# Performance work log

Measured on AMD Instinct MI355X. Metric: run time of the kernel, lower is better.

## Reference

```python
import jax, jax.numpy as jnp
import numpy as np

B, S, IN_DIM, OUT_DIM = 4, 2048, 1024, 1024
NEG = -9e15

def _xavier(key, shape, gain=1.414):
    fan_in, fan_out = shape[0], shape[1]
    a = gain * np.sqrt(6.0 / (fan_in + fan_out))
    return jax.random.uniform(key, shape, jnp.float32, -a, a)

def setup_inputs() -> dict:
    key = jax.random.key(0)
    ks = jax.random.split(key, 8)
    x = jax.random.normal(ks[0], (B, S, IN_DIM), jnp.float32)
    W_query = _xavier(ks[1], (IN_DIM, OUT_DIM))
    W_key = _xavier(ks[2], (IN_DIM, OUT_DIM))
    W_value = _xavier(ks[3], (IN_DIM, OUT_DIM))
    # torch Linear default init (kaiming-uniform-ish); values don't matter for correctness baseline
    W1 = _xavier(ks[4], (OUT_DIM + IN_DIM, OUT_DIM), gain=1.0)
    b1 = jnp.zeros((OUT_DIM,), jnp.float32)
    W2 = _xavier(ks[5], (OUT_DIM, OUT_DIM), gain=1.0)
    b2 = jnp.zeros((OUT_DIM,), jnp.float32)
    return {"x": x, "W_query": W_query, "W_key": W_key, "W_value": W_value,
            "W1": W1, "b1": b1, "W2": W2, "b2": b2}

def reference(x, W_query, W_key, W_value, W1, b1, W2, b2):
    # QKV projections: [B,S,in] @ [in,out] -> [B,S,out]
    q = jnp.einsum('bsi,io->bso', x, W_query)
    k = jnp.einsum('bsi,io->bso', x, W_key)
    v = jnp.einsum('bsi,io->bso', x, W_value)
    scale = 1.0 / jnp.sqrt(jnp.float32(OUT_DIM))
    e = jnp.einsum('bqd,bkd->bqk', q, k) * scale  # [B,S,S]
    causal = jnp.tril(jnp.ones((S, S), jnp.float32))  # mask > 0 keeps lower triangle
    attn = jnp.where(causal > 0, e, jnp.float32(NEG))
    attn = jax.nn.softmax(attn, axis=2)
    # dropout: eval mode (train=False) -> identity
    out = jnp.einsum('bqk,bkd->bqd', attn, v)  # [B,S,out]
    h = jnp.concatenate([out, x], axis=-1)  # [B,S,out+in]
    h = jax.nn.relu(jnp.einsum('bsf,fo->bso', h, W1) + b1)
    return jnp.einsum('bsf,fo->bso', h, W2) + b2
```

## Files before the change

kernel.cpp:

```cpp
#include <hip/hip_runtime.h>
#include <stdint.h>

typedef __attribute__((ext_vector_type(8))) short short8;
typedef __attribute__((ext_vector_type(4))) short short4v;
typedef __attribute__((ext_vector_type(4))) float f32x4;

__device__ __forceinline__ unsigned short f32_to_bf16(float f) {
    unsigned int u = __float_as_uint(f);
    u += 0x7FFFu + ((u >> 16) & 1u);
    return (unsigned short)(u >> 16);
}

__device__ __forceinline__ short8 load8_f32_as_bf16(const float* __restrict__ ap) {
    f32x4 f0 = *(const f32x4*)ap;
    f32x4 f1 = *(const f32x4*)(ap + 4);
    union { short8 s; unsigned short u[8]; } cv;
#pragma unroll
    for (int t = 0; t < 4; ++t) {
        cv.u[t]     = f32_to_bf16(f0[t]);
        cv.u[t + 4] = f32_to_bf16(f1[t]);
    }
    return cv.s;
}

__device__ __forceinline__ void gld_lds16(const void* g, void* l) {
    __builtin_amdgcn_global_load_lds(
        (const __attribute__((address_space(1))) unsigned int*)(unsigned long long)(uintptr_t)g,
        (__attribute__((address_space(3))) unsigned int*)(unsigned int)(uintptr_t)l,
        16, 0, 0);
}

template<int EPI, int SWIZ, int MT>
__global__ __launch_bounds__(256, 4)
void gemm128(const unsigned short* __restrict__ A,
             int lda,
             const unsigned short* __restrict__ B, int ldb,
             void* __restrict__ C, int ldc, int K,
             long bStride, long cStride,
             void* __restrict__ C2, int ldc2)
{
    int z = blockIdx.z;
    int mblk, nblk;
    {
        int x = blockIdx.x, yy = blockIdx.y;
        if (z < 2) { mblk = x * 8 + (yy & 7); nblk = yy >> 3; }
        else       { nblk = x * 8 + (yy & 7); mblk = yy >> 3; }
    }
    int m0 = mblk * MT;
    int n0 = nblk * 128;

    const unsigned short* Ab;
    const unsigned short* Bb;
    if (z < 2) { Ab = A; Bb = B + (size_t)z * bStride; }
    else       { Ab = B + (size_t)2 * bStride; Bb = A; }

    __shared__ __align__(16) short As[MT * 64];
    __shared__ __align__(16) short Bs[128 * 64];

    int tid  = threadIdx.x;
    int lane = tid & 63, wid = tid >> 6;
    constexpr int MI = MT / 32;
    int wm = (wid & 1) * (MT / 2), wn = (wid >> 1) * 64;
    int fr = lane & 15, fq = lane >> 4;
    int sw0 = ((fq    ) ^ (fr & 7)) * 16;
    int sw1 = ((fq ^ 4) ^ (fr & 7)) * 16;

    int rS = tid >> 3;
    int cS = ((tid & 7) ^ (rS & 7)) * 8;
    char* AsB = (char*)As; char* BsB = (char*)Bs;

    f32x4 acc[MI][4];
#pragma unroll
    for (int i = 0; i < MI; ++i)
#pragma unroll
    for (int j = 0; j < 4; ++j) acc[i][j] = f32x4{0.f, 0.f, 0.f, 0.f};

    for (int k0 = 0; k0 < K; k0 += 64) {
        const unsigned short* pa = Ab + (size_t)(m0 + rS) * lda + k0 + cS;
        const unsigned short* pb = Bb + (size_t)(n0 + rS) * ldb + k0 + cS;
#pragma unroll
        for (int t = 0; t < MT / 32; ++t)
            gld_lds16(pa + (size_t)(32 * t) * lda, AsB + t * 4096 + tid * 16);
#pragma unroll
        for (int t = 0; t < 4; ++t)
            gld_lds16(pb + (size_t)(32 * t) * ldb,  BsB + t * 4096 + tid * 16);
        __syncthreads();

#pragma unroll
        for (int kh = 0; kh < 2; ++kh) {
            int sw = kh ? sw1 : sw0;
            short8 a[MI], b[4];
#pragma unroll
            for (int i = 0; i < MI; ++i)
                a[i] = *(const short8*)(AsB + (wm + i * 16 + fr) * 128 + sw);
#pragma unroll
            for (int j = 0; j < 4; ++j)
                b[j] = *(const short8*)(BsB + (wn + j * 16 + fr) * 128 + sw);
#pragma unroll
            for (int i = 0; i < MI; ++i)
#pragma unroll
            for (int j = 0; j < 4; ++j)
                acc[i][j] = __builtin_amdgcn_mfma_f32_16x16x32_bf16(a[i], b[j], acc[i][j], 0, 0, 0);
        }
        __syncthreads();
    }

    unsigned short* Cz; int ldcz;
    if (z >= 2) { Cz = (unsigned short*)C2; ldcz = ldc2; }
    else { Cz = (unsigned short*)C + (size_t)z * cStride; ldcz = ldc; }
#pragma unroll
    for (int i = 0; i < MI; ++i)
#pragma unroll
    for (int j = 0; j < 4; ++j)
#pragma unroll
    for (int r = 0; r < 4; ++r) {
        int row = m0 + wm + i * 16 + fq * 4 + r;
        int col = n0 + wn + j * 16 + fr;
        Cz[(size_t)row * ldcz + col] = f32_to_bf16(acc[i][j][r]);
    }
}

template<int AMODE, int EPI, int SWIZ, bool KLIMIT>
__global__ __launch_bounds__(512, 2)
void gemm8p(const unsigned short* __restrict__ A, const unsigned short* __restrict__ A2,
            int lda, int lda2, int ksplit,
            const unsigned short* __restrict__ B, int ldb,
            void* __restrict__ C, int ldc, int K,
            long aStride, long bStride, long cStride,
            const float* __restrict__ bias, long biasStride, float scale)
{
    int z = blockIdx.z;
    int mblk, nblk;
    if (SWIZ == 1) {
        int lin = blockIdx.y * gridDim.x + blockIdx.x;
        int xcd = lin & 7, idx = lin >> 3;
        int mch = (int)gridDim.y >> 3;
        mblk = xcd * mch + idx % mch;
        nblk = idx / mch;
    } else if (SWIZ == 5) {
        int x = blockIdx.x;
        int i = 0;
        while (i < 7 && (i + 1) * (i + 2) <= x) ++i;
        mblk = i;
        nblk = x - i * (i + 1);
    } else if (SWIZ == 8) {
        int p = blockIdx.x;
        int s = (int)blockIdx.z * 8 + (int)blockIdx.y;
        nblk = s >> 2;
        int msel = (s >> 1) & 1, zsel = s & 1;
        z    = 2 * (p & 1) + zsel;
        mblk = msel ? 7 - (p >> 1) : (p >> 1);
    } else {
        mblk = blockIdx.y;
        nblk = blockIdx.x;
    }
    int m0 = mblk * 256, n0 = nblk * 128;

    const unsigned short* Ab = A + (size_t)z * aStride;
    const unsigned short* Bb = B + (size_t)z * bStride;

    constexpr int TILE = 49152;
    __shared__ __align__(16) char lds[3 * TILE];

    int tid  = threadIdx.x;
    int lane = tid & 63, wid = tid >> 6;
    int wm = (wid & 3) * 64, wn = (wid >> 2) * 64;
    int fr = lane & 15, fq = lane >> 4;
    int sw0 = ((fq    ) ^ (fr & 7)) * 16;
    int sw1 = ((fq ^ 4) ^ (fr & 7)) * 16;

    int rS = tid >> 3;
    int cS = ((tid & 7) ^ (rS & 7)) * 8;

    int kend = KLIMIT ? min(K, m0 + 256) : K;
    int NT = kend >> 6;

    f32x4 acc[4][4];
#pragma unroll
    for (int i = 0; i < 4; ++i)
#pragma unroll
    for (int j = 0; j < 4; ++j) acc[i][j] = f32x4{0.f, 0.f, 0.f, 0.f};

    auto STAGE = [&](int t, int slot) {
        int k0 = t << 6;
        char* dst = lds + slot * TILE;
        const unsigned short* Asrc = Ab; int koff = k0, ldax = lda;
        if (AMODE == 2 && k0 >= ksplit) { Asrc = A2; koff = k0 - ksplit; ldax = lda2; }
        const unsigned short* pa = Asrc + (size_t)(m0 + rS) * ldax + koff + cS;
        const unsigned short* pb = Bb   + (size_t)(n0 + rS) * ldb  + k0   + cS;
#pragma unroll
        for (int u = 0; u < 4; ++u)
            gld_lds16(pa + (size_t)(64 * u) * ldax, dst + u * 8192 + tid * 16);
#pragma unroll
        for (int u = 0; u < 2; ++u)
            gld_lds16(pb + (size_t)(64 * u) * ldb, dst + 32768 + u * 8192 + tid * 16);
    };

    STAGE(0, 0);
    STAGE(1, 1);
    asm volatile("s_waitcnt vmcnt(6)" ::: "memory");
    __builtin_amdgcn_s_barrier();
    __builtin_amdgcn_sched_barrier(0);
    asm volatile("" ::: "memory");

    int sc = 0, ss = 2;
    for (int t = 0; t < NT; ++t) {
        if (t + 2 < NT) STAGE(t + 2, ss);
        const char* AsB = (const char*)(lds + sc * TILE);
        const char* BsB = AsB + 32768;
#pragma unroll
        for (int kh = 0; kh < 2; ++kh) {
            int sw = kh ? sw1 : sw0;
            short8 a[4], b[4];
#pragma unroll
            for (int i = 0; i < 4; ++i)
                a[i] = *(const short8*)(AsB + (wm + i * 16 + fr) * 128 + sw);
#pragma unroll
            for (int j = 0; j < 4; ++j)
                b[j] = *(const short8*)(BsB + (wn + j * 16 + fr) * 128 + sw);
            __builtin_amdgcn_s_setprio(1);
#pragma unroll
            for (int i = 0; i < 4; ++i)
#pragma unroll
            for (int j = 0; j < 4; ++j)
                acc[i][j] = __builtin_amdgcn_mfma_f32_16x16x32_bf16(a[i], b[j], acc[i][j], 0, 0, 0);
            __builtin_amdgcn_s_setprio(0);
        }
        if (t + 1 < NT) {
            if (t + 2 < NT) { asm volatile("s_waitcnt vmcnt(6)" ::: "memory"); }
            else            { asm volatile("s_waitcnt vmcnt(0)" ::: "memory"); }
            __builtin_amdgcn_s_barrier();
            __builtin_amdgcn_sched_barrier(0);
            asm volatile("" ::: "memory");
        }
        sc = sc == 2 ? 0 : sc + 1;
        ss = ss == 2 ? 0 : ss + 1;
    }

    if (EPI == 6) {
        unsigned short* Cz = (unsigned short*)C + (size_t)z * cStride;
        float* rs = const_cast<float*>(bias) + z * biasStride;
#pragma unroll
        for (int i = 0; i < 4; ++i)
#pragma unroll
        for (int r = 0; r < 4; ++r) {
            int row = m0 + wm + i * 16 + fq * 4 + r;
            float s = 0.f;
#pragma unroll
            for (int j = 0; j < 4; ++j) {
                int col = n0 + wn + j * 16 + fr;
                float e = (col <= row) ? __expf(acc[i][j][r] * scale - 16.f) : 0.f;
                s += e;
                Cz[(size_t)row * ldc + col] = f32_to_bf16(e);
            }
            s += __shfl_xor(s, 1);
            s += __shfl_xor(s, 2);
            s += __shfl_xor(s, 4);
            s += __shfl_xor(s, 8);
            if (fr == 0) atomicAdd(&rs[row], s);
        }
    } else if (EPI == 4) {
        unsigned short* Cz = (unsigned short*)C + (size_t)z * cStride;
#pragma unroll
        for (int i = 0; i < 4; ++i)
#pragma unroll
        for (int r = 0; r < 4; ++r) {
            int row = m0 + wm + i * 16 + fq * 4 + r;
            float inv = 1.f / bias[z * biasStride + row];
#pragma unroll
            for (int j = 0; j < 4; ++j) {
                int col = n0 + wn + j * 16 + fr;
                Cz[(size_t)row * ldc + col] = f32_to_bf16(acc[i][j][r] * inv);
            }
        }
    } else {
#pragma unroll
        for (int i = 0; i < 4; ++i)
#pragma unroll
        for (int j = 0; j < 4; ++j)
#pragma unroll
        for (int r = 0; r < 4; ++r) {
            int row = m0 + wm + i * 16 + fq * 4 + r;
            int col = n0 + wn + j * 16 + fr;
            float v = acc[i][j][r];
            if (EPI == 2) {
                v += bias[col];
                v = v > 0.f ? v : 0.f;
                ((unsigned short*)C)[(size_t)row * ldc + col] = f32_to_bf16(v);
            } else {
                ((float*)C)[(size_t)row * ldc + col] = v + bias[col];
            }
        }
    }
}

__device__ __forceinline__ void transpose_tile64(const float* __restrict__ in,
                                                 unsigned short* __restrict__ out,
                                                 int rows, int cols, int bx, int by, int tid)
{
    __shared__ float t[64][65];
    int tx = tid & 15, ty = tid >> 4;
    int r0 = by * 64, c0 = bx * 64;
#pragma unroll
    for (int i = 0; i < 4; ++i) {
        f32x4 v = *(const f32x4*)(in + (size_t)(r0 + ty + i * 16) * cols + c0 + tx * 4);
#pragma unroll
        for (int j = 0; j < 4; ++j) t[ty + i * 16][tx * 4 + j] = v[j];
    }
    __syncthreads();
#pragma unroll
    for (int i = 0; i < 4; ++i) {
        union { short4v s; unsigned short u[4]; } o;
#pragma unroll
        for (int j = 0; j < 4; ++j) o.u[j] = f32_to_bf16(t[tx * 4 + j][ty + i * 16]);
        *(short4v*)(out + (size_t)(c0 + ty + i * 16) * rows + r0 + tx * 4) = o.s;
    }
}

__global__ __launch_bounds__(256)
void prep_kernel(const float* __restrict__ x,
                 const float* __restrict__ Wq, const float* __restrict__ Wk,
                 const float* __restrict__ Wv, const float* __restrict__ W1,
                 const float* __restrict__ W2,
                 unsigned short* __restrict__ xb, unsigned short* __restrict__ WT,
                 unsigned short* __restrict__ W1T, unsigned short* __restrict__ W2T,
                 float* __restrict__ rsum)
{
    int idx = blockIdx.x;
    int tid = threadIdx.x;
    if (idx < 1024) {
#pragma unroll
        for (int it = 0; it < 4; ++it) {
            size_t i = ((size_t)idx * 4 + it) * 2048 + (size_t)tid * 8;
            *(short8*)(xb + i) = load8_f32_as_bf16(x + i);
        }
    } else if (idx < 1792) {
        int t = idx - 1024;
        int w = t >> 8; t &= 255;
        const float* in = w == 0 ? Wq : (w == 1 ? Wk : Wv);
        transpose_tile64(in, WT + (size_t)w * 1024 * 1024, 1024, 1024,
                         t & 15, t >> 4, tid);
    } else if (idx < 2304) {
        int t = idx - 1792;
        transpose_tile64(W1, W1T, 2048, 1024, t & 15, t >> 4, tid);
    } else if (idx < 2560) {
        int t = idx - 2304;
        transpose_tile64(W2, W2T, 1024, 1024, t & 15, t >> 4, tid);
    } else {
        int t = idx - 2560;
        f32x4 zero = {0.f, 0.f, 0.f, 0.f};
        float* p = rsum + ((size_t)t * 256 + tid) * 8;
        *(f32x4*)p = zero;
        *(f32x4*)(p + 4) = zero;
    }
}

extern "C" void kernel_launch(void* const* d_in, const int* in_sizes, int n_in,
                              void* d_out, int out_size, void* d_ws, size_t ws_size,
                              hipStream_t stream)
{
    const float* x  = (const float*)d_in[0];
    const float* Wq = (const float*)d_in[1];
    const float* Wk = (const float*)d_in[2];
    const float* Wv = (const float*)d_in[3];
    const float* W1 = (const float*)d_in[4];
    const float* b1 = (const float*)d_in[5];
    const float* W2 = (const float*)d_in[6];
    const float* b2 = (const float*)d_in[7];
    float* out = (float*)d_out;

    size_t off = 0;
    auto alloc = [&](size_t bytes) {
        char* r = (char*)d_ws + off;
        off += (bytes + 255) & ~(size_t)255;
        return r;
    };
    const size_t TOK = (size_t)8192 * 1024;
    unsigned short* WT   = (unsigned short*)alloc((size_t)3072 * 1024 * 2);
    unsigned short* W1T  = (unsigned short*)alloc((size_t)1024 * 2048 * 2);
    unsigned short* W2T  = (unsigned short*)alloc((size_t)1024 * 1024 * 2);
    unsigned short* xb   = (unsigned short*)alloc(TOK * 2);
    unsigned short* vT   = (unsigned short*)alloc((size_t)1024 * 8192 * 2);
    unsigned short* attn = (unsigned short*)alloc(TOK * 2);
    float*          rsum = (float*)         alloc((size_t)4 * 2048 * 4);
    unsigned short* q    = (unsigned short*)alloc(TOK * 2);
    unsigned short* k    = (unsigned short*)alloc(TOK * 2);
    unsigned short* S    = (unsigned short*)alloc((size_t)4 * 2048 * 2048 * 2);
    unsigned short* h1   = S;

    prep_kernel<<<2564, 256, 0, stream>>>(x, Wq, Wk, Wv, W1, W2, xb, WT, W1T, W2T, rsum);

    gemm128<0, 6, 128><<<dim3(8, 64, 3), 256, 0, stream>>>(
        xb, 1024, WT, 1024, q, 1024, 1024,
        (long)1024 * 1024, (long)TOK, vT, 8192);

    gemm8p<0, 6, 5, false><<<dim3(72, 1, 4), 512, 0, stream>>>(
        q, nullptr, 1024, 0, 0, k, 1024, S, 2048, 1024,
        (long)2048 * 1024, (long)2048 * 1024, (long)2048 * 2048,
        rsum, 2048, 0.03125f);

    gemm8p<0, 4, 8, true><<<dim3(8, 8, 4), 512, 0, stream>>>(
        S, nullptr, 2048, 0, 0, vT, 8192, attn, 1024, 2048,
        (long)2048 * 2048, (long)2048, (long)2048 * 1024,
        rsum, 2048, 0.f);

    gemm8p<2, 2, 1, false><<<dim3(8, 32, 1), 512, 0, stream>>>(
        attn, xb, 1024, 1024, 1024, W1T, 2048, h1, 1024, 2048,
        0, 0, 0, b1, 0, 0.f);

    gemm8p<0, 3, 1, false><<<dim3(8, 32, 1), 512, 0, stream>>>(
        h1, nullptr, 1024, 0, 0, W2T, 1024, out, 1024, 1024,
        0, 0, 0, b2, 0, 0.f);
}
```

Baseline: 293.9 us.

## Use 128x128 double-buffered tiles for causal attention GEMMs with XCD-aware scheduling

New measurement: 285.4 us. 2.9% less time.

```diff
diff --git a/kernel.cpp b/kernel.cpp
--- a/kernel.cpp
+++ b/kernel.cpp
@@ -30,7 +30,7 @@
         16, 0, 0);
 }
 
-template<int EPI, int SWIZ, int MT>
+template<int MT>
 __global__ __launch_bounds__(256, 4)
 void gemm128(const unsigned short* __restrict__ A,
              int lda,
@@ -120,10 +120,10 @@
     }
 }
 
-template<int AMODE, int EPI, int SWIZ, bool KLIMIT>
-__global__ __launch_bounds__(512, 2)
-void gemm8p(const unsigned short* __restrict__ A, const unsigned short* __restrict__ A2,
-            int lda, int lda2, int ksplit,
+template<int EPI, int SWIZ, bool KLIMIT>
+__global__ __launch_bounds__(256, 2)
+void gemmdb(const unsigned short* __restrict__ A,
+            int lda,
             const unsigned short* __restrict__ B, int ldb,
             void* __restrict__ C, int ldc, int K,
             long aStride, long bStride, long cStride,
@@ -131,40 +131,40 @@
 {
     int z = blockIdx.z;
     int mblk, nblk;
-    if (SWIZ == 1) {
-        int lin = blockIdx.y * gridDim.x + blockIdx.x;
-        int xcd = lin & 7, idx = lin >> 3;
-        int mch = (int)gridDim.y >> 3;
-        mblk = xcd * mch + idx % mch;
-        nblk = idx / mch;
-    } else if (SWIZ == 5) {
+    if (SWIZ == 5) {
         int x = blockIdx.x;
-        int i = 0;
-        while (i < 7 && (i + 1) * (i + 2) <= x) ++i;
-        mblk = i;
-        nblk = x - i * (i + 1);
-    } else if (SWIZ == 8) {
-        int p = blockIdx.x;
-        int s = (int)blockIdx.z * 8 + (int)blockIdx.y;
-        nblk = s >> 2;
-        int msel = (s >> 1) & 1, zsel = s & 1;
-        z    = 2 * (p & 1) + zsel;
-        mblk = msel ? 7 - (p >> 1) : (p >> 1);
+        int per = (int)gridDim.x >> 3;
+        x = (x & 7) * per + (x >> 3);
+        int a = (int)sqrtf(2.f * (float)x + 1.f);
+        if (a > 15) a = 15;
+        while (a < 15 && ((a + 1) * (a + 2) / 2) <= x) ++a;
+        while (a > 0 && (a * (a + 1) / 2) > x) --a;
+        mblk = a;
+        nblk = x - a * (a + 1) / 2;
+    } else if (SWIZ == 7) {
+        int glin = (int)blockIdx.z * 128 + (int)blockIdx.y * 8 + (int)blockIdx.x;
+        int xcd = glin & 7;
+        int s   = glin >> 3;
+        z = xcd >> 1;
+        int h  = xcd & 1;
+        int jm = s & 7;
+        nblk   = s >> 3;
+        mblk   = (jm & 1) ? (15 - h - (jm >> 1) * 2) : ((jm >> 1) * 2 + h);
     } else {
         mblk = blockIdx.y;
         nblk = blockIdx.x;
     }
-    int m0 = mblk * 256, n0 = nblk * 128;
+    int m0 = mblk * 128;
+    int n0 = nblk * 128;
 
     const unsigned short* Ab = A + (size_t)z * aStride;
     const unsigned short* Bb = B + (size_t)z * bStride;
 
-    constexpr int TILE = 49152;
-    __shared__ __align__(16) char lds[3 * TILE];
+    __shared__ __align__(16) char lds[65536];
 
     int tid  = threadIdx.x;
     int lane = tid & 63, wid = tid >> 6;
-    int wm = (wid & 3) * 64, wn = (wid >> 2) * 64;
+    int wm = (wid & 1) * 64, wn = (wid >> 1) * 64;
     int fr = lane & 15, fq = lane >> 4;
     int sw0 = ((fq    ) ^ (fr & 7)) * 16;
     int sw1 = ((fq ^ 4) ^ (fr & 7)) * 16;
@@ -172,7 +172,7 @@
     int rS = tid >> 3;
     int cS = ((tid & 7) ^ (rS & 7)) * 8;
 
-    int kend = KLIMIT ? min(K, m0 + 256) : K;
+    int kend = KLIMIT ? min(K, m0 + 128) : K;
     int NT = kend >> 6;
 
     f32x4 acc[4][4];
@@ -181,33 +181,30 @@
 #pragma unroll
     for (int j = 0; j < 4; ++j) acc[i][j] = f32x4{0.f, 0.f, 0.f, 0.f};
 
-    auto STAGE = [&](int t, int slot) {
-        int k0 = t << 6;
-        char* dst = lds + slot * TILE;
-        const unsigned short* Asrc = Ab; int koff = k0, ldax = lda;
-        if (AMODE == 2 && k0 >= ksplit) { Asrc = A2; koff = k0 - ksplit; ldax = lda2; }
-        const unsigned short* pa = Asrc + (size_t)(m0 + rS) * ldax + koff + cS;
-        const unsigned short* pb = Bb   + (size_t)(n0 + rS) * ldb  + k0   + cS;
+    auto STAGE = [&](int kt) {
+        char* dst = lds + (kt & 1) * 32768;
+        const unsigned short* pa = Ab + (size_t)(m0 + rS) * lda + (kt << 6) + cS;
+        const unsigned short* pb = Bb + (size_t)(n0 + rS) * ldb + (kt << 6) + cS;
 #pragma unroll
         for (int u = 0; u < 4; ++u)
-            gld_lds16(pa + (size_t)(64 * u) * ldax, dst + u * 8192 + tid * 16);
-#pragma unroll
-        for (int u = 0; u < 2; ++u)
-            gld_lds16(pb + (size_t)(64 * u) * ldb, dst + 32768 + u * 8192 + tid * 16);
+            gld_lds16(pa + (size_t)(32 * u) * lda, dst + u * 4096 + tid * 16);
+#pragma unroll
+        for (int u = 0; u < 4; ++u)
+            gld_lds16(pb + (size_t)(32 * u) * ldb, dst + 16384 + u * 4096 + tid * 16);
     };
 
-    STAGE(0, 0);
-    STAGE(1, 1);
-    asm volatile("s_waitcnt vmcnt(6)" ::: "memory");
-    __builtin_amdgcn_s_barrier();
-    __builtin_amdgcn_sched_barrier(0);
-    asm volatile("" ::: "memory");
-
-    int sc = 0, ss = 2;
+    STAGE(0);
     for (int t = 0; t < NT; ++t) {
-        if (t + 2 < NT) STAGE(t + 2, ss);
-        const char* AsB = (const char*)(lds + sc * TILE);
-        const char* BsB = AsB + 32768;
+        if (t + 1 < NT) {
+            STAGE(t + 1);
+            asm volatile("s_waitcnt vmcnt(8)" ::: "memory");
+        } else {
+            asm volatile("s_waitcnt vmcnt(0)" ::: "memory");
+        }
+        __builtin_amdgcn_s_barrier();
+        __builtin_amdgcn_sched_barrier(0);
+        const char* AsB = (const char*)lds + (t & 1) * 32768;
+        const char* BsB = AsB + 16384;
 #pragma unroll
         for (int kh = 0; kh < 2; ++kh) {
             int sw = kh ? sw1 : sw0;
@@ -226,15 +223,9 @@
                 acc[i][j] = __builtin_amdgcn_mfma_f32_16x16x32_bf16(a[i], b[j], acc[i][j], 0, 0, 0);
             __builtin_amdgcn_s_setprio(0);
         }
-        if (t + 1 < NT) {
-            if (t + 2 < NT) { asm volatile("s_waitcnt vmcnt(6)" ::: "memory"); }
-            else            { asm volatile("s_waitcnt vmcnt(0)" ::: "memory"); }
-            __builtin_amdgcn_s_barrier();
-            __builtin_amdgcn_sched_barrier(0);
-            asm volatile("" ::: "memory");
-        }
-        sc = sc == 2 ? 0 : sc + 1;
-        ss = ss == 2 ? 0 : ss + 1;
+        __builtin_amdgcn_s_barrier();
+        __builtin_amdgcn_sched_barrier(0);
+        asm volatile("" ::: "memory");
     }
 
     if (EPI == 6) {
@@ -259,7 +250,7 @@
             s += __shfl_xor(s, 8);
             if (fr == 0) atomicAdd(&rs[row], s);
         }
-    } else if (EPI == 4) {
+    } else {
         unsigned short* Cz = (unsigned short*)C + (size_t)z * cStride;
 #pragma unroll
         for (int i = 0; i < 4; ++i)
@@ -273,23 +264,116 @@
                 Cz[(size_t)row * ldc + col] = f32_to_bf16(acc[i][j][r] * inv);
             }
         }
-    } else {
-#pragma unroll
-        for (int i = 0; i < 4; ++i)
-#pragma unroll
-        for (int j = 0; j < 4; ++j)
-#pragma unroll
-        for (int r = 0; r < 4; ++r) {
-            int row = m0 + wm + i * 16 + fq * 4 + r;
-            int col = n0 + wn + j * 16 + fr;
-            float v = acc[i][j][r];
-            if (EPI == 2) {
-                v += bias[col];
-                v = v > 0.f ? v : 0.f;
-                ((unsigned short*)C)[(size_t)row * ldc + col] = f32_to_bf16(v);
-            } else {
-                ((float*)C)[(size_t)row * ldc + col] = v + bias[col];
-            }
+    }
+}
+
+template<int AMODE, int EPI>
+__global__ __launch_bounds__(512, 2)
+void gemm8p(const unsigned short* __restrict__ A, const unsigned short* __restrict__ A2,
+            int lda, int lda2, int ksplit,
+            const unsigned short* __restrict__ B, int ldb,
+            void* __restrict__ C, int ldc, int K,
+            const float* __restrict__ bias)
+{
+    int lin = blockIdx.y * gridDim.x + blockIdx.x;
+    int xcd = lin & 7, idx = lin >> 3;
+    int mch = (int)gridDim.y >> 3;
+    int mblk = xcd * mch + idx % mch;
+    int nblk = idx / mch;
+    int m0 = mblk * 256, n0 = nblk * 128;
+
+    constexpr int TILE = 49152;
+    __shared__ __align__(16) char lds[3 * TILE];
+
+    int tid  = threadIdx.x;
+    int lane = tid & 63, wid = tid >> 6;
+    int wm = (wid & 3) * 64, wn = (wid >> 2) * 64;
+    int fr = lane & 15, fq = lane >> 4;
+    int sw0 = ((fq    ) ^ (fr & 7)) * 16;
+    int sw1 = ((fq ^ 4) ^ (fr & 7)) * 16;
+
+    int rS = tid >> 3;
+    int cS = ((tid & 7) ^ (rS & 7)) * 8;
+
+    int NT = K >> 6;
+
+    f32x4 acc[4][4];
+#pragma unroll
+    for (int i = 0; i < 4; ++i)
+#pragma unroll
+    for (int j = 0; j < 4; ++j) acc[i][j] = f32x4{0.f, 0.f, 0.f, 0.f};
+
+    auto STAGE = [&](int t, int slot) {
+        int k0 = t << 6;
+        char* dst = lds + slot * TILE;
+        const unsigned short* Asrc = A; int koff = k0, ldax = lda;
+        if (AMODE == 2 && k0 >= ksplit) { Asrc = A2; koff = k0 - ksplit; ldax = lda2; }
+        const unsigned short* pa = Asrc + (size_t)(m0 + rS) * ldax + koff + cS;
+        const unsigned short* pb = B    + (size_t)(n0 + rS) * ldb  + k0   + cS;
+#pragma unroll
+        for (int u = 0; u < 4; ++u)
+            gld_lds16(pa + (size_t)(64 * u) * ldax, dst + u * 8192 + tid * 16);
+#pragma unroll
+        for (int u = 0; u < 2; ++u)
+            gld_lds16(pb + (size_t)(64 * u) * ldb, dst + 32768 + u * 8192 + tid * 16);
+    };
+
+    STAGE(0, 0);
+    STAGE(1, 1);
+    asm volatile("s_waitcnt vmcnt(6)" ::: "memory");
+    __builtin_amdgcn_s_barrier();
+    __builtin_amdgcn_sched_barrier(0);
+    asm volatile("" ::: "memory");
+
+    int sc = 0, ss = 2;
+    for (int t = 0; t < NT; ++t) {
+        if (t + 2 < NT) STAGE(t + 2, ss);
+        const char* AsB = (const char*)(lds + sc * TILE);
+        const char* BsB = AsB + 32768;
+#pragma unroll
+        for (int kh = 0; kh < 2; ++kh) {
+            int sw = kh ? sw1 : sw0;
+            short8 a[4], b[4];
+#pragma unroll
+            for (int i = 0; i < 4; ++i)
+                a[i] = *(const short8*)(AsB + (wm + i * 16 + fr) * 128 + sw);
+#pragma unroll
+            for (int j = 0; j < 4; ++j)
+                b[j] = *(const short8*)(BsB + (wn + j * 16 + fr) * 128 + sw);
+            __builtin_amdgcn_s_setprio(1);
+#pragma unroll
+            for (int i = 0; i < 4; ++i)
+#pragma unroll
+            for (int j = 0; j < 4; ++j)
+                acc[i][j] = __builtin_amdgcn_mfma_f32_16x16x32_bf16(a[i], b[j], acc[i][j], 0, 0, 0);
+            __builtin_amdgcn_s_setprio(0);
+        }
+        if (t + 1 < NT) {
+            if (t + 2 < NT) { asm volatile("s_waitcnt vmcnt(6)" ::: "memory"); }
+            else            { asm volatile("s_waitcnt vmcnt(0)" ::: "memory"); }
+            __builtin_amdgcn_s_barrier();
+            __builtin_amdgcn_sched_barrier(0);
+            asm volatile("" ::: "memory");
+        }
+        sc = sc == 2 ? 0 : sc + 1;
+        ss = ss == 2 ? 0 : ss + 1;
+    }
+
+#pragma unroll
+    for (int i = 0; i < 4; ++i)
+#pragma unroll
+    for (int j = 0; j < 4; ++j)
+#pragma unroll
+    for (int r = 0; r < 4; ++r) {
+        int row = m0 + wm + i * 16 + fq * 4 + r;
+        int col = n0 + wn + j * 16 + fr;
+        float v = acc[i][j][r];
+        if (EPI == 2) {
+            v += bias[col];
+            v = v > 0.f ? v : 0.f;
+            ((unsigned short*)C)[(size_t)row * ldc + col] = f32_to_bf16(v);
+        } else {
+            ((float*)C)[(size_t)row * ldc + col] = v + bias[col];
         }
     }
 }
@@ -390,25 +474,21 @@
 
     prep_kernel<<<2564, 256, 0, stream>>>(x, Wq, Wk, Wv, W1, W2, xb, WT, W1T, W2T, rsum);
 
-    gemm128<0, 6, 128><<<dim3(8, 64, 3), 256, 0, stream>>>(
+    gemm128<128><<<dim3(8, 64, 3), 256, 0, stream>>>(
         xb, 1024, WT, 1024, q, 1024, 1024,
         (long)1024 * 1024, (long)TOK, vT, 8192);
 
-    gemm8p<0, 6, 5, false><<<dim3(72, 1, 4), 512, 0, stream>>>(
-        q, nullptr, 1024, 0, 0, k, 1024, S, 2048, 1024,
-        (long)2048 * 1024, (long)2048 * 1024, (long)2048 * 2048,
-        rsum, 2048, 0.03125f);
-
-    gemm8p<0, 4, 8, true><<<dim3(8, 8, 4), 512, 0, stream>>>(
-        S, nullptr, 2048, 0, 0, vT, 8192, attn, 1024, 2048,
-        (long)2048 * 2048, (long)2048, (long)2048 * 1024,
-        rsum, 2048, 0.f);
-
-    gemm8p<2, 2, 1, false><<<dim3(8, 32, 1), 512, 0, stream>>>(
-        attn, xb, 1024, 1024, 1024, W1T, 2048, h1, 1024, 2048,
-        0, 0, 0, b1, 0, 0.f);
-
-    gemm8p<0, 3, 1, false><<<dim3(8, 32, 1), 512, 0, stream>>>(
-        h1, nullptr, 1024, 0, 0, W2T, 1024, out, 1024, 1024,
-        0, 0, 0, b2, 0, 0.f);
-}
+    gemmdb<6, 5, false><<<dim3(136, 1, 4), 256, 0, stream>>>(
+        q, 1024, k, 1024, S, 2048, 1024,
+        (long)2048 * 1024, (long)2048 * 1024, (long)2048 * 2048, rsum, 2048, 0.03125f);
+
+    gemmdb<4, 7, true><<<dim3(8, 16, 4), 256, 0, stream>>>(
+        S, 2048, vT, 8192, attn, 1024, 2048,
+        (long)2048 * 2048, (long)2048, (long)2048 * 1024, rsum, 2048, 0.f);
+
+    gemm8p<2, 2><<<dim3(8, 32, 1), 512, 0, stream>>>(
+        attn, xb, 1024, 1024, 1024, W1T, 2048, h1, 1024, 2048, b1);
+
+    gemm8p<0, 3><<<dim3(8, 32, 1), 512, 0, stream>>>(
+        h1, nullptr, 1024, 0, 0, W2T, 1024, out, 1024, 1024, b2);
+}
```
